# Performance work log

Hardware: AMD Instinct MI355X
Metric: run time of the kernel (lower is better)

Reference implementation:

```python
import jax, jax.numpy as jnp
import numpy as np

HEADS = 16
EMBED = 1024
HEAD_DIM = EMBED // HEADS


def setup_inputs() -> dict:
    k = jax.random.key(0)
    ks = jax.random.split(k, 8)
    N, L = 8, 1024
    s = 1.0 / np.sqrt(HEAD_DIM)
    return {
        "key": jax.random.normal(ks[0], (N, L, EMBED), jnp.float32),
        "query": jax.random.normal(ks[1], (N, L, EMBED), jnp.float32),
        "value": jax.random.normal(ks[2], (N, L, EMBED), jnp.float32),
        "mask": jnp.ones((N, 1, 1, L), jnp.int32),
        "Wq": jax.random.normal(ks[3], (HEAD_DIM, HEAD_DIM), jnp.float32) * s,
        "Wk": jax.random.normal(ks[4], (HEAD_DIM, HEAD_DIM), jnp.float32) * s,
        "Wv": jax.random.normal(ks[5], (HEAD_DIM, HEAD_DIM), jnp.float32) * s,
        "Wo": jax.random.normal(ks[6], (EMBED, EMBED), jnp.float32) * (1.0 / np.sqrt(EMBED)),
    }


def reference(key, query, value, mask, Wq, Wk, Wv, Wo):
    # NOTE: original torch code calls weights.masked_fill(...) without assignment,
    # which is a no-op, so `mask` is faithfully ignored here.
    N, Lq, E = query.shape
    Lk = key.shape[1]
    H, D = HEADS, E // HEADS
    q = query.reshape(N, Lq, H, D)
    k = key.reshape(N, Lk, H, D)
    v = value.reshape(N, Lk, H, D)
    # per-head linear with weight shared across heads: x @ W^T (torch Linear)
    q = jnp.einsum('nqhd,ed->nqhe', q, Wq)
    k = jnp.einsum('nkhd,ed->nkhe', k, Wk)
    v = jnp.einsum('nkhd,ed->nkhe', v, Wv)
    weights = jnp.einsum('nqhd,nkhd->nhqk', q, k)
    attn = jax.nn.softmax(weights / jnp.sqrt(jnp.asarray(E, weights.dtype)), axis=-1)
    out = jnp.einsum('nhqk,nkhd->nqhd', attn, v).reshape(N, Lq, E)
    return out @ Wo.T
```

## Files before the change

kernel.cpp:

```cpp
#include <hip/hip_runtime.h>
#include <hip/hip_bf16.h>

#define HEADS 16
#define HDIM  64
#define EMB   1024
#define NB    8
#define SEQ   1024

typedef __bf16 bf16_t;
typedef __bf16 bf16x8 __attribute__((ext_vector_type(8)));
typedef __bf16 bf16x4 __attribute__((ext_vector_type(4)));
typedef float  floatx4 __attribute__((ext_vector_type(4)));

union PkU { unsigned u; __bf16 h[2]; };

__device__ __forceinline__ bf16x8 load8bf(const bf16_t* p) { return *(const bf16x8*)p; }
__device__ __forceinline__ bf16x4 cvt4(float4 a) {
    bf16x4 r; r[0]=(bf16_t)a.x; r[1]=(bf16_t)a.y; r[2]=(bf16_t)a.z; r[3]=(bf16_t)a.w;
    return r;
}
__device__ __forceinline__ bf16x8 cvt8(float4 a, float4 b) {
    bf16x8 r;
    r[0]=(bf16_t)a.x; r[1]=(bf16_t)a.y; r[2]=(bf16_t)a.z; r[3]=(bf16_t)a.w;
    r[4]=(bf16_t)b.x; r[5]=(bf16_t)b.y; r[6]=(bf16_t)b.z; r[7]=(bf16_t)b.w;
    return r;
}

__global__ __launch_bounds__(256) void proj_kernel(
    const float* __restrict__ q_in, const float* __restrict__ k_in,
    const float* __restrict__ v_in,
    const float* __restrict__ Wq, const float* __restrict__ Wk,
    const float* __restrict__ Wv,
    bf16_t* __restrict__ qp, bf16_t* __restrict__ kp, bf16_t* __restrict__ vt)
{
    __shared__ __align__(16) bf16_t wl[64][72];
    __shared__ __align__(16) bf16_t lo[64][72];

    const int wave = threadIdx.x >> 6;
    const int lane = threadIdx.x & 63;
    const int m  = lane & 15;
    const int q4 = lane >> 4;
    const int op = blockIdx.y;

    const float* x = (op == 0) ? q_in : (op == 1) ? k_in : v_in;
    const float* W = (op == 0) ? Wq   : (op == 1) ? Wk   : Wv;

    {
        const int t  = threadIdx.x;
        const int f  = t >> 2;
        const int kg = (t & 3) * 16;
        #pragma unroll
        for (int j = 0; j < 4; ++j) {
            float4 v = *(const float4*)(W + f * 64 + kg + j * 4);
            *(bf16x4*)&wl[f][kg + j * 4] = cvt4(v);
        }
    }
    __syncthreads();

    if (op == 2) {
        const int nh = blockIdx.x >> 4;
        const int l0 = (blockIdx.x & 15) * 64;
        const int n  = nh >> 4;
        const int h  = nh & 15;

        const int la = l0 + wave * 16 + m;
        const float* xr = x + (size_t)(n * 16384 + la * 16 + h) * 64;
        float4 f0 = *(const float4*)(xr + q4 * 8);
        float4 f1 = *(const float4*)(xr + q4 * 8 + 4);
        float4 f2 = *(const float4*)(xr + 32 + q4 * 8);
        float4 f3 = *(const float4*)(xr + 32 + q4 * 8 + 4);
        bf16x8 a0 = cvt8(f0, f1);
        bf16x8 a1 = cvt8(f2, f3);

        floatx4 acc[4];
        #pragma unroll
        for (int sub = 0; sub < 4; ++sub) {
            bf16x8 b0 = load8bf(&wl[sub * 16 + m][q4 * 8]);
            bf16x8 b1 = load8bf(&wl[sub * 16 + m][32 + q4 * 8]);
            floatx4 z = {0.f, 0.f, 0.f, 0.f};
            z = __builtin_amdgcn_mfma_f32_16x16x32_bf16(a0, b0, z, 0, 0, 0);
            z = __builtin_amdgcn_mfma_f32_16x16x32_bf16(a1, b1, z, 0, 0, 0);
            acc[sub] = z;
        }

        #pragma unroll
        for (int sub = 0; sub < 4; ++sub) {
            #pragma unroll
            for (int r = 0; r < 4; r += 2) {
                PkU u; u.h[0] = (bf16_t)acc[sub][r]; u.h[1] = (bf16_t)acc[sub][r + 1];
                *(unsigned*)&lo[sub * 16 + m][wave * 16 + q4 * 4 + r] = u.u;
            }
        }
        __syncthreads();

        const int e  = threadIdx.x >> 2;
        const int lc = (threadIdx.x & 3) * 16;
        bf16_t* dst = vt + ((size_t)nh * 64 + e) * 1024 + l0 + lc;
        *(bf16x8*)dst       = *(const bf16x8*)&lo[e][lc];
        *(bf16x8*)(dst + 8) = *(const bf16x8*)&lo[e][lc + 8];
    } else {
        const int row0 = blockIdx.x * 64 + wave * 16;

        const float* xr = x + (size_t)(row0 + m) * 64;
        float4 f0 = *(const float4*)(xr + q4 * 8);
        float4 f1 = *(const float4*)(xr + q4 * 8 + 4);
        float4 f2 = *(const float4*)(xr + 32 + q4 * 8);
        float4 f3 = *(const float4*)(xr + 32 + q4 * 8 + 4);
        bf16x8 a0 = cvt8(f0, f1);
        bf16x8 a1 = cvt8(f2, f3);

        floatx4 acc[4];
        #pragma unroll
        for (int sub = 0; sub < 4; ++sub) {
            bf16x8 b0 = load8bf(&wl[sub * 16 + m][q4 * 8]);
            bf16x8 b1 = load8bf(&wl[sub * 16 + m][32 + q4 * 8]);
            floatx4 z = {0.f, 0.f, 0.f, 0.f};
            z = __builtin_amdgcn_mfma_f32_16x16x32_bf16(a0, b0, z, 0, 0, 0);
            z = __builtin_amdgcn_mfma_f32_16x16x32_bf16(a1, b1, z, 0, 0, 0);
            acc[sub] = z;
        }

        #pragma unroll
        for (int sub = 0; sub < 4; ++sub) {
            #pragma unroll
            for (int r = 0; r < 4; ++r) {
                lo[wave * 16 + q4 * 4 + r][sub * 16 + m] = (bf16_t)acc[sub][r];
            }
        }
        __syncthreads();

        const int gl = threadIdx.x >> 2;
        const int ec = (threadIdx.x & 3) * 16;
        const int g  = blockIdx.x * 64 + gl;
        const int n  = g >> 14;
        const int l  = (g >> 4) & 1023;
        const int h  = g & 15;
        const int nh = n * 16 + h;
        bf16_t* dst = ((op == 0) ? qp : kp) + ((size_t)nh * 1024 + l) * 64 + ec;
        *(bf16x8*)dst       = *(const bf16x8*)&lo[gl][ec];
        *(bf16x8*)(dst + 8) = *(const bf16x8*)&lo[gl][ec + 8];
    }
}

__global__ __launch_bounds__(256) void attn_kernel(
    bf16_t* __restrict__ qp, const bf16_t* __restrict__ kp,
    const bf16_t* __restrict__ vt)
{
    __shared__ __align__(16) bf16_t kl[2][64][64];
    __shared__ __align__(16) bf16_t vl[2][64][64];

    const int lane = threadIdx.x & 63;
    const int wave = threadIdx.x >> 6;
    const int m  = lane & 15;
    const int q4 = lane >> 4;

    const int nh   = blockIdx.x & 127;
    const int qblk = blockIdx.x >> 7;

    bf16_t* Q = qp + (size_t)nh * 65536;
    const bf16_t* K = kp + (size_t)nh * 65536;
    const bf16_t* V = vt + (size_t)nh * 65536;

    const int qb = qblk * 64 + wave * 16;

    const int srow  = lane >> 3;
    const int sslot = lane & 7;
    const int ch    = sslot ^ srow;

    auto stage = [&](int b, int kb) {
        #pragma unroll
        for (int i = 0; i < 2; ++i) {
            const int rbase = wave * 16 + i * 8;
            const int row   = rbase + srow;
            __builtin_amdgcn_global_load_lds(
                (const __attribute__((address_space(1))) unsigned int*)(K + (size_t)(kb + row) * 64 + ch * 8),
                (__attribute__((address_space(3))) unsigned int*)(&kl[b][rbase][0]),
                16, 0, 0);
            __builtin_amdgcn_global_load_lds(
                (const __attribute__((address_space(1))) unsigned int*)(V + (size_t)row * 1024 + kb + ch * 8),
                (__attribute__((address_space(3))) unsigned int*)(&vl[b][rbase][0]),
                16, 0, 0);
        }
    };

    stage(0, 0);

    bf16x8 bqa = load8bf(Q + (qb + m) * 64 + q4 * 8);
    bf16x8 bqb = load8bf(Q + (qb + m) * 64 + 32 + q4 * 8);

    floatx4 o[4];
    #pragma unroll
    for (int i = 0; i < 4; ++i) o[i] = (floatx4){0.f, 0.f, 0.f, 0.f};
    float lsum = 0.f;
    const float CE = 1.4426950408889634f * 0.03125f;

    const int c0 = (q4 ^ (m & 7)) * 8;
    const int c1 = ((q4 + 4) ^ (m & 7)) * 8;
    const int hsel = q4 >> 1;

    int cur = 0;
    __syncthreads();

    for (int kt = 0; kt < 16; ++kt) {
        if (kt < 15) stage(cur ^ 1, (kt + 1) * 64);

        floatx4 s[4];
        __builtin_amdgcn_s_setprio(1);
        #pragma unroll
        for (int sk = 0; sk < 4; ++sk) {
            bf16x8 ka0 = load8bf(&kl[cur][sk * 16 + m][c0]);
            bf16x8 ka1 = load8bf(&kl[cur][sk * 16 + m][c1]);
            floatx4 z = {0.f, 0.f, 0.f, 0.f};
            z = __builtin_amdgcn_mfma_f32_16x16x32_bf16(ka0, bqa, z, 0, 0, 0);
            z = __builtin_amdgcn_mfma_f32_16x16x32_bf16(ka1, bqb, z, 0, 0, 0);
            s[sk] = z;
        }
        __builtin_amdgcn_s_setprio(0);

        unsigned pk[2][4];
        #pragma unroll
        for (int c = 0; c < 2; ++c) {
            #pragma unroll
            for (int r = 0; r < 4; ++r) {
                float a0 = exp2f(s[2 * c][r] * CE);
                float a1 = exp2f(s[2 * c + 1][r] * CE);
                lsum += a0 + a1;
                PkU u; u.h[0] = (bf16_t)a0; u.h[1] = (bf16_t)a1;
                pk[c][r] = u.u;
            }
        }

        bf16x8 va[8];
        #pragma unroll
        for (int sd = 0; sd < 4; ++sd) {
            va[2 * sd]     = load8bf(&vl[cur][sd * 16 + m][c0]);
            va[2 * sd + 1] = load8bf(&vl[cur][sd * 16 + m][c1]);
        }

        bf16x8 bp[2];
        #pragma unroll
        for (int c = 0; c < 2; ++c) {
            #pragma unroll
            for (int j = 0; j < 8; ++j) {
                const int src = m + 16 * ((2 * q4 + (j >> 2)) & 3);
                PkU u; u.u = (unsigned)__shfl((int)pk[c][j & 3], src, 64);
                bp[c][j] = u.h[hsel];
            }
        }

        __builtin_amdgcn_s_setprio(1);
        #pragma unroll
        for (int sd = 0; sd < 4; ++sd) {
            o[sd] = __builtin_amdgcn_mfma_f32_16x16x32_bf16(va[2 * sd],     bp[0], o[sd], 0, 0, 0);
            o[sd] = __builtin_amdgcn_mfma_f32_16x16x32_bf16(va[2 * sd + 1], bp[1], o[sd], 0, 0, 0);
        }
        __builtin_amdgcn_s_setprio(0);

        __syncthreads();
        cur ^= 1;
    }

    lsum += __shfl_xor(lsum, 16, 64); lsum += __shfl_xor(lsum, 32, 64);
    const float inv = 1.0f / lsum;

    #pragma unroll
    for (int sd = 0; sd < 4; ++sd) {
        bf16x4 w;
        #pragma unroll
        for (int r = 0; r < 4; ++r) w[r] = (bf16_t)(o[sd][r] * inv);
        *(bf16x4*)(Q + (size_t)(qb + m) * 64 + sd * 16 + q4 * 4) = w;
    }
}

__global__ __launch_bounds__(256) void wocvt_kernel(
    const float* __restrict__ Wo, bf16_t* __restrict__ wo_bf)
{
    const int i = (blockIdx.x * 256 + threadIdx.x) * 8;
    float4 f0 = *(const float4*)(Wo + i);
    float4 f1 = *(const float4*)(Wo + i + 4);
    *(bf16x8*)(wo_bf + i) = cvt8(f0, f1);
}

__global__ __launch_bounds__(256) void outproj_kernel(
    const bf16_t* __restrict__ aoq, const bf16_t* __restrict__ wo_bf,
    float* __restrict__ out)
{
    __shared__ __align__(16) bf16_t wl[128][72];

    const int wave = threadIdx.x >> 6;
    const int lane = threadIdx.x & 63;
    const int m  = lane & 15;
    const int q4 = lane >> 4;

    const int bx = blockIdx.x >> 3;
    const int by = blockIdx.x & 7;

    const int row0 = bx * 128 + wave * 32;
    const int col0 = by * 128;

    const int ts_f = threadIdx.x >> 1;
    const int ts_k = (threadIdx.x & 1) * 32;

    floatx4 acc[2][8];
    #pragma unroll
    for (int rs = 0; rs < 2; ++rs)
        #pragma unroll
        for (int cs = 0; cs < 8; ++cs) acc[rs][cs] = (floatx4){0.f, 0.f, 0.f, 0.f};

    for (int h = 0; h < 16; ++h) {
        const int kc = h * 64;
        __syncthreads();
        #pragma unroll
        for (int j = 0; j < 4; ++j) {
            *(bf16x8*)&wl[ts_f][ts_k + j * 8] =
                load8bf(wo_bf + (size_t)(col0 + ts_f) * 1024 + kc + ts_k + j * 8);
        }
        __syncthreads();

        bf16x8 a[2][2];
        #pragma unroll
        for (int rs = 0; rs < 2; ++rs) {
            const int g = row0 + rs * 16 + m;
            const int n = g >> 10;
            const int q = g & 1023;
            const bf16_t* arow = aoq + ((size_t)(n * 16 + h) * 1024 + q) * 64;
            a[rs][0] = load8bf(arow + q4 * 8);
            a[rs][1] = load8bf(arow + 32 + q4 * 8);
        }

        #pragma unroll
        for (int cs = 0; cs < 8; ++cs) {
            bf16x8 b0 = load8bf(&wl[cs * 16 + m][q4 * 8]);
            bf16x8 b1 = load8bf(&wl[cs * 16 + m][32 + q4 * 8]);
            #pragma unroll
            for (int rs = 0; rs < 2; ++rs) {
                acc[rs][cs] = __builtin_amdgcn_mfma_f32_16x16x32_bf16(a[rs][0], b0, acc[rs][cs], 0, 0, 0);
                acc[rs][cs] = __builtin_amdgcn_mfma_f32_16x16x32_bf16(a[rs][1], b1, acc[rs][cs], 0, 0, 0);
            }
        }
    }

    #pragma unroll
    for (int rs = 0; rs < 2; ++rs) {
        #pragma unroll
        for (int r = 0; r < 4; ++r) {
            const int g = row0 + rs * 16 + q4 * 4 + r;
            #pragma unroll
            for (int cs = 0; cs < 8; ++cs)
                out[(size_t)g * 1024 + col0 + cs * 16 + m] = acc[rs][cs][r];
        }
    }
}

extern "C" void kernel_launch(void* const* d_in, const int* in_sizes, int n_in,
                              void* d_out, int out_size, void* d_ws, size_t ws_size,
                              hipStream_t stream) {
    const float* key   = (const float*)d_in[0];
    const float* query = (const float*)d_in[1];
    const float* value = (const float*)d_in[2];
    const float* Wq = (const float*)d_in[4];
    const float* Wk = (const float*)d_in[5];
    const float* Wv = (const float*)d_in[6];
    const float* Wo = (const float*)d_in[7];

    const size_t TENS = (size_t)NB * SEQ * EMB;
    bf16_t* qp = (bf16_t*)d_ws;
    bf16_t* vt = qp + TENS;
    bf16_t* kp = (bf16_t*)d_out;

    hipLaunchKernelGGL(proj_kernel, dim3(2048, 3), dim3(256), 0, stream,
                       query, key, value, Wq, Wk, Wv, qp, kp, vt);
    hipLaunchKernelGGL(attn_kernel, dim3(2048), dim3(256), 0, stream, qp, kp, vt);
    hipLaunchKernelGGL(wocvt_kernel, dim3(512), dim3(256), 0, stream, Wo, vt);
    hipLaunchKernelGGL(outproj_kernel, dim3(512), dim3(256), 0, stream,
                       qp, vt, (float*)d_out);
}
```

Before: 301.0 us.

## Switch attention to 32x32x16 MFMA with 32 query rows per wave

```diff
diff --git a/kernel.cpp b/kernel.cpp
--- a/kernel.cpp
+++ b/kernel.cpp
@@ -11,8 +11,10 @@
 typedef __bf16 bf16x8 __attribute__((ext_vector_type(8)));
 typedef __bf16 bf16x4 __attribute__((ext_vector_type(4)));
 typedef float  floatx4 __attribute__((ext_vector_type(4)));
+typedef float  f32x16  __attribute__((ext_vector_type(16)));
 
 union PkU { unsigned u; __bf16 h[2]; };
+union W4U { unsigned u[4]; bf16x8 v; };
 
 __device__ __forceinline__ bf16x8 load8bf(const bf16_t* p) { return *(const bf16x8*)p; }
 __device__ __forceinline__ bf16x4 cvt4(float4 a) {
@@ -151,8 +153,8 @@
 
     const int lane = threadIdx.x & 63;
     const int wave = threadIdx.x >> 6;
-    const int m  = lane & 15;
-    const int q4 = lane >> 4;
+    const int q32  = lane & 31;
+    const int hi   = lane >> 5;
 
     const int nh   = blockIdx.x & 127;
     const int qblk = blockIdx.x >> 7;
@@ -161,7 +163,7 @@
     const bf16_t* K = kp + (size_t)nh * 65536;
     const bf16_t* V = vt + (size_t)nh * 65536;
 
-    const int qb = qblk * 64 + wave * 16;
+    const int qb = qblk * 128 + wave * 32;
 
     const int srow  = lane >> 3;
     const int sslot = lane & 7;
@@ -185,90 +187,96 @@
 
     stage(0, 0);
 
-    bf16x8 bqa = load8bf(Q + (qb + m) * 64 + q4 * 8);
-    bf16x8 bqb = load8bf(Q + (qb + m) * 64 + 32 + q4 * 8);
-
-    floatx4 o[4];
+    bf16x8 bq[4];
     #pragma unroll
-    for (int i = 0; i < 4; ++i) o[i] = (floatx4){0.f, 0.f, 0.f, 0.f};
+    for (int sl = 0; sl < 4; ++sl)
+        bq[sl] = load8bf(Q + (size_t)(qb + q32) * 64 + sl * 16 + hi * 8);
+
+    f32x16 o0 = {0.f,0.f,0.f,0.f,0.f,0.f,0.f,0.f,0.f,0.f,0.f,0.f,0.f,0.f,0.f,0.f};
+    f32x16 o1 = o0;
     float lsum = 0.f;
     const float CE = 1.4426950408889634f * 0.03125f;
 
-    const int c0 = (q4 ^ (m & 7)) * 8;
-    const int c1 = ((q4 + 4) ^ (m & 7)) * 8;
-    const int hsel = q4 >> 1;
-
     int cur = 0;
     __syncthreads();
 
     for (int kt = 0; kt < 16; ++kt) {
         if (kt < 15) stage(cur ^ 1, (kt + 1) * 64);
 
-        floatx4 s[4];
-        __builtin_amdgcn_s_setprio(1);
-        #pragma unroll
-        for (int sk = 0; sk < 4; ++sk) {
-            bf16x8 ka0 = load8bf(&kl[cur][sk * 16 + m][c0]);
-            bf16x8 ka1 = load8bf(&kl[cur][sk * 16 + m][c1]);
-            floatx4 z = {0.f, 0.f, 0.f, 0.f};
-            z = __builtin_amdgcn_mfma_f32_16x16x32_bf16(ka0, bqa, z, 0, 0, 0);
-            z = __builtin_amdgcn_mfma_f32_16x16x32_bf16(ka1, bqb, z, 0, 0, 0);
-            s[sk] = z;
-        }
-        __builtin_amdgcn_s_setprio(0);
-
-        unsigned pk[2][4];
-        #pragma unroll
-        for (int c = 0; c < 2; ++c) {
-            #pragma unroll
-            for (int r = 0; r < 4; ++r) {
-                float a0 = exp2f(s[2 * c][r] * CE);
-                float a1 = exp2f(s[2 * c + 1][r] * CE);
-                lsum += a0 + a1;
-                PkU u; u.h[0] = (bf16_t)a0; u.h[1] = (bf16_t)a1;
-                pk[c][r] = u.u;
-            }
-        }
-
-        bf16x8 va[8];
-        #pragma unroll
-        for (int sd = 0; sd < 4; ++sd) {
-            va[2 * sd]     = load8bf(&vl[cur][sd * 16 + m][c0]);
-            va[2 * sd + 1] = load8bf(&vl[cur][sd * 16 + m][c1]);
-        }
-
-        bf16x8 bp[2];
-        #pragma unroll
-        for (int c = 0; c < 2; ++c) {
-            #pragma unroll
-            for (int j = 0; j < 8; ++j) {
-                const int src = m + 16 * ((2 * q4 + (j >> 2)) & 3);
-                PkU u; u.u = (unsigned)__shfl((int)pk[c][j & 3], src, 64);
-                bp[c][j] = u.h[hsel];
-            }
-        }
-
-        __builtin_amdgcn_s_setprio(1);
-        #pragma unroll
-        for (int sd = 0; sd < 4; ++sd) {
-            o[sd] = __builtin_amdgcn_mfma_f32_16x16x32_bf16(va[2 * sd],     bp[0], o[sd], 0, 0, 0);
-            o[sd] = __builtin_amdgcn_mfma_f32_16x16x32_bf16(va[2 * sd + 1], bp[1], o[sd], 0, 0, 0);
-        }
-        __builtin_amdgcn_s_setprio(0);
+        #pragma unroll
+        for (int kb32 = 0; kb32 < 2; ++kb32) {
+            const int krow = kb32 * 32 + q32;
+            f32x16 s = {0.f,0.f,0.f,0.f,0.f,0.f,0.f,0.f,0.f,0.f,0.f,0.f,0.f,0.f,0.f,0.f};
+            __builtin_amdgcn_s_setprio(1);
+            #pragma unroll
+            for (int sl = 0; sl < 4; ++sl) {
+                const int ck = ((sl * 2 + hi) ^ (krow & 7)) * 8;
+                bf16x8 ka = load8bf(&kl[cur][krow][ck]);
+                s = __builtin_amdgcn_mfma_f32_32x32x16_bf16(ka, bq[sl], s, 0, 0, 0);
+            }
+            __builtin_amdgcn_s_setprio(0);
+
+            unsigned w[8];
+            #pragma unroll
+            for (int t = 0; t < 8; ++t) {
+                float p0 = exp2f(s[2 * t]     * CE);
+                float p1 = exp2f(s[2 * t + 1] * CE);
+                lsum += p0 + p1;
+                PkU u; u.h[0] = (bf16_t)p0; u.h[1] = (bf16_t)p1;
+                w[t] = u.u;
+            }
+
+            bf16x8 va[4];
+            #pragma unroll
+            for (int db = 0; db < 2; ++db) {
+                const int d = db * 32 + q32;
+                #pragma unroll
+                for (int c = 0; c < 2; ++c) {
+                    const int cv = ((kb32 * 4 + c * 2 + hi) ^ (d & 7)) * 8;
+                    va[db * 2 + c] = load8bf(&vl[cur][d][cv]);
+                }
+            }
+
+            const unsigned e0 = (unsigned)__shfl_xor((int)(hi ? w[0] : w[2]), 32, 64);
+            const unsigned e1 = (unsigned)__shfl_xor((int)(hi ? w[1] : w[3]), 32, 64);
+            const unsigned e2 = (unsigned)__shfl_xor((int)(hi ? w[4] : w[6]), 32, 64);
+            const unsigned e3 = (unsigned)__shfl_xor((int)(hi ? w[5] : w[7]), 32, 64);
+
+            W4U b0v, b1v;
+            b0v.u[0] = hi ? e0 : w[0];
+            b0v.u[1] = hi ? e1 : w[1];
+            b0v.u[2] = hi ? w[2] : e0;
+            b0v.u[3] = hi ? w[3] : e1;
+            b1v.u[0] = hi ? e2 : w[4];
+            b1v.u[1] = hi ? e3 : w[5];
+            b1v.u[2] = hi ? w[6] : e2;
+            b1v.u[3] = hi ? w[7] : e3;
+
+            __builtin_amdgcn_s_setprio(1);
+            o0 = __builtin_amdgcn_mfma_f32_32x32x16_bf16(va[0], b0v.v, o0, 0, 0, 0);
+            o0 = __builtin_amdgcn_mfma_f32_32x32x16_bf16(va[1], b1v.v, o0, 0, 0, 0);
+            o1 = __builtin_amdgcn_mfma_f32_32x32x16_bf16(va[2], b0v.v, o1, 0, 0, 0);
+            o1 = __builtin_amdgcn_mfma_f32_32x32x16_bf16(va[3], b1v.v, o1, 0, 0, 0);
+            __builtin_amdgcn_s_setprio(0);
+        }
 
         __syncthreads();
         cur ^= 1;
     }
 
-    lsum += __shfl_xor(lsum, 16, 64); lsum += __shfl_xor(lsum, 32, 64);
+    lsum += __shfl_xor(lsum, 32, 64);
     const float inv = 1.0f / lsum;
 
     #pragma unroll
-    for (int sd = 0; sd < 4; ++sd) {
-        bf16x4 w;
-        #pragma unroll
-        for (int r = 0; r < 4; ++r) w[r] = (bf16_t)(o[sd][r] * inv);
-        *(bf16x4*)(Q + (size_t)(qb + m) * 64 + sd * 16 + q4 * 4) = w;
+    for (int g = 0; g < 4; ++g) {
+        bf16x4 w0v, w1v;
+        #pragma unroll
+        for (int r = 0; r < 4; ++r) {
+            w0v[r] = (bf16_t)(o0[g * 4 + r] * inv);
+            w1v[r] = (bf16_t)(o1[g * 4 + r] * inv);
+        }
+        *(bf16x4*)(Q + (size_t)(qb + q32) * 64 +      g * 8 + hi * 4) = w0v;
+        *(bf16x4*)(Q + (size_t)(qb + q32) * 64 + 32 + g * 8 + hi * 4) = w1v;
     }
 }
 
@@ -370,7 +378,7 @@
 
     hipLaunchKernelGGL(proj_kernel, dim3(2048, 3), dim3(256), 0, stream,
                        query, key, value, Wq, Wk, Wv, qp, kp, vt);
-    hipLaunchKernelGGL(attn_kernel, dim3(2048), dim3(256), 0, stream, qp, kp, vt);
+    hipLaunchKernelGGL(attn_kernel, dim3(1024), dim3(256), 0, stream, qp, kp, vt);
     hipLaunchKernelGGL(wocvt_kernel, dim3(512), dim3(256), 0, stream, Wo, vt);
     hipLaunchKernelGGL(outproj_kernel, dim3(512), dim3(256), 0, stream,
                        qp, vt, (float*)d_out);
```

Result: faster. 264.8 us (-12.0%).
